# Kernel optimization log

Hardware: AMD Instinct MI355X
Metric: run time of the kernel (lower is better)

## Reference

```python
import jax, jax.numpy as jnp
import numpy as np

DELTA = 0.05
STOP = 10
INV_DELTA = 1.0 / DELTA
TOTAL = int(STOP * INV_DELTA)  # 200 bins
# slice_vol = arange(delta/2, stop, delta)**1 * delta * 2*pi*3
SLICE_VOL = (np.arange(DELTA / 2, STOP, DELTA) * DELTA * 2.0 * np.pi * 3.0).astype(np.float32)


def _cdist(a, b):
    # Euclidean pairwise distance [Na, Nb] via the (a-b)^2 = a^2 + b^2 - 2ab identity
    a2 = jnp.sum(a * a, axis=-1)
    b2 = jnp.sum(b * b, axis=-1)
    d2 = a2[:, None] + b2[None, :] - 2.0 * (a @ b.T)
    return jnp.sqrt(jnp.maximum(d2, 0.0))


def _pair_hist(pa, pb, same, real_size, vol):
    # integer distance bins; torch .int() truncates, distances are >= 0 so floor is equivalent
    bins = jnp.floor(_cdist(pa * real_size, pb * real_size) * INV_DELTA).astype(jnp.int32)
    if same:
        n = pa.shape[0]
        idx = jnp.arange(n)
        bins = bins.at[idx, idx].set(9999)  # fill_diagonal_(9999) -> excluded self-pairs
    valid = (bins < TOTAL).astype(jnp.float32).ravel()  # mask: bins beyond stop dropped
    counts = jnp.zeros(TOTAL, jnp.float32).at[jnp.clip(bins, 0, TOTAL - 1).ravel()].add(valid)
    density = pb.shape[0] / vol
    return counts / density / jnp.asarray(SLICE_VOL) / pa.shape[0]


def setup_inputs() -> dict:
    key = jax.random.key(0)
    k0, k1 = jax.random.split(key)
    pos0 = jax.random.uniform(k0, (4096, 3), dtype=jnp.float32)
    pos1 = jax.random.uniform(k1, (8192, 3), dtype=jnp.float32)
    count = jnp.zeros((2, 2, TOTAL), dtype=jnp.float32)
    real_size = jnp.array([25.0, 25.0, 3.0], dtype=jnp.float32)
    return {"pos0": pos0, "pos1": pos1, "count": count, "real_size": real_size}


def reference(pos0, pos1, count, real_size):
    vol = real_size[0] * real_size[1] * real_size[2]
    pos = [pos0, pos1]
    bufs = [
        jnp.stack([_pair_hist(pos[i], pos[j], i == j, real_size, vol) for j in range(2)])
        for i in range(2)
    ]
    # count buffer is accumulated in-place in torch; return the updated buffer
    return count + jnp.stack(bufs)
```

## Files before the change

kernel.cpp:

```cpp
#include <hip/hip_runtime.h>
#include <math.h>

#define TOTAL 200
#define TB    32
#define BLK   256
#define NW    4
#define GRID  2048
#define NR    16
#define RATIO (BLK/TB)

typedef float f32x4 __attribute__((ext_vector_type(4)));

__global__ void rdf_prep(const float* __restrict__ p0, const float* __restrict__ p1,
                         const float* __restrict__ rs,
                         float4* __restrict__ b0, float4* __restrict__ b1,
                         unsigned int* __restrict__ ghist, int n0, int n1)
{
    const float sx = rs[0], sy = rs[1], sz = rs[2];
    int t = blockIdx.x * blockDim.x + threadIdx.x;
    if (t < n0) {
        float x = p0[t*3+0]*sx, y = p0[t*3+1]*sy, z = p0[t*3+2]*sz;
        b0[t] = make_float4(x, y, z, x*x + y*y + z*z);
    } else if (t < n0 + n1) {
        int u = t - n0;
        float x = p1[u*3+0]*sx, y = p1[u*3+1]*sy, z = p1[u*3+2]*sz;
        b1[u] = make_float4(x, y, z, x*x + y*y + z*z);
    }
    if (t < NR * 3 * TOTAL) ghist[t] = 0;
}

template<bool DIAG>
__device__ __forceinline__ void pair_one(f32x4 q, int J,
                                         float ax, float ay, float az, float a2,
                                         unsigned int* __restrict__ mylh, int ofs)
{
    float dot = ax*q.x + ay*q.y + az*q.z;
    float d2  = (a2 + q.w) - 2.0f*dot;
    float v   = __builtin_amdgcn_sqrtf(fmaxf(d2, 0.0f)) * 20.0f;
    bool ok   = (v < 200.0f);
    if (DIAG) ok = ok && (J > ofs);
    if (ok) atomicAdd(&mylh[(int)v], 1u);
}

template<bool DIAG>
__device__ __forceinline__ void pair_loop(const f32x4* __restrict__ Bb, int colBase,
                                          float ax, float ay, float az, float a2,
                                          unsigned int* __restrict__ mylh, int ofs)
{
    unsigned voff = (unsigned)colBase * 16u;
    #pragma unroll
    for (int jb = 0; jb < TB; jb += 8) {
        f32x4 q0, q1, q2, q3, q4, q5, q6, q7;
        asm volatile(
            "global_load_dwordx4 %0, %8, %9 offset:0\n\t"
            "global_load_dwordx4 %1, %8, %9 offset:16\n\t"
            "global_load_dwordx4 %2, %8, %9 offset:32\n\t"
            "global_load_dwordx4 %3, %8, %9 offset:48\n\t"
            "global_load_dwordx4 %4, %8, %9 offset:64\n\t"
            "global_load_dwordx4 %5, %8, %9 offset:80\n\t"
            "global_load_dwordx4 %6, %8, %9 offset:96\n\t"
            "global_load_dwordx4 %7, %8, %9 offset:112\n\t"
            "s_waitcnt vmcnt(0)"
            : "=&v"(q0), "=&v"(q1), "=&v"(q2), "=&v"(q3),
              "=&v"(q4), "=&v"(q5), "=&v"(q6), "=&v"(q7)
            : "v"(voff), "s"(Bb));
        pair_one<DIAG>(q0, jb+0, ax, ay, az, a2, mylh, ofs);
        pair_one<DIAG>(q1, jb+1, ax, ay, az, a2, mylh, ofs);
        pair_one<DIAG>(q2, jb+2, ax, ay, az, a2, mylh, ofs);
        pair_one<DIAG>(q3, jb+3, ax, ay, az, a2, mylh, ofs);
        pair_one<DIAG>(q4, jb+4, ax, ay, az, a2, mylh, ofs);
        pair_one<DIAG>(q5, jb+5, ax, ay, az, a2, mylh, ofs);
        pair_one<DIAG>(q6, jb+6, ax, ay, az, a2, mylh, ofs);
        pair_one<DIAG>(q7, jb+7, ax, ay, az, a2, mylh, ofs);
        __builtin_amdgcn_sched_barrier(0);
        voff += 128u;
    }
}

__global__ __launch_bounds__(BLK, 8) void rdf_hist(
    const float4* __restrict__ b0, const float4* __restrict__ b1,
    unsigned int* __restrict__ ghist,
    int n0, int n1, int T0, int T01, int Ttot,
    int cb0, int cb1, int rows0, int rows1)
{
    __shared__ unsigned int lh[3][NW][2][TOTAL];

    const int tid  = threadIdx.x;
    const int wave = tid >> 6;
    const int par  = tid & 1;

    uint4* z = (uint4*)lh;
    for (int k = tid; k < 3*NW*2*TOTAL/4; k += BLK) z[k] = make_uint4(0,0,0,0);
    __syncthreads();

    const int gBeg = (int)(((long long)blockIdx.x       * Ttot) / GRID);
    const int gEnd = (int)(((long long)(blockIdx.x + 1) * Ttot) / GRID);

    for (int g = gBeg; g < gEnd; ++g) {
        int type, rb, cb;
        if (g < T0) {
            type = 0; rb = 0;
            while (rb + 1 < rows0 && (cb0*(rb+1) - (RATIO/2)*(rb+1)*rb) <= g) ++rb;
            cb = RATIO*rb + (g - (cb0*rb - (RATIO/2)*rb*(rb-1)));
        } else if (g < T01) {
            int u = g - T0; type = 1; rb = u / cb1; cb = u - rb*cb1;
        } else {
            int u = g - T01; type = 2; rb = 0;
            while (rb + 1 < rows1 && (cb1*(rb+1) - (RATIO/2)*(rb+1)*rb) <= u) ++rb;
            cb = RATIO*rb + (u - (cb1*rb - (RATIO/2)*rb*(rb-1)));
        }
        const float4* Ab = (type == 2) ? b1 : b0;
        const float4* Bb = (type == 0) ? b0 : b1;
        const int nA     = (type == 2) ? n1 : n0;

        const int rowBase = rb * BLK;
        const int colBase = cb * TB;
        const int aIdx    = rowBase + tid;

        float4 a = (aIdx < nA) ? Ab[aIdx]
                               : make_float4(0.f, 0.f, 0.f, 3.0e18f);
        unsigned int* mylh = &lh[type][wave][par][0];
        const f32x4* Bb4   = (const f32x4*)Bb;

        const bool diag = (type != 1) && (colBase < rowBase + BLK);
        if (diag) pair_loop<true >(Bb4, colBase, a.x, a.y, a.z, a.w, mylh, aIdx - colBase);
        else      pair_loop<false>(Bb4, colBase, a.x, a.y, a.z, a.w, mylh, 0);
    }
    __syncthreads();

    unsigned int* gh = ghist + (blockIdx.x & (NR - 1)) * (3 * TOTAL);
    for (int k = tid; k < 3 * TOTAL; k += BLK) {
        int type = k / TOTAL, bin = k - type * TOTAL;
        unsigned int c = 0;
        #pragma unroll
        for (int w = 0; w < NW; ++w)
            { c += lh[type][w][0][bin] + lh[type][w][1][bin]; }
        if (c) atomicAdd(&gh[k], (type == 1) ? c : 2u * c);
    }
}

__global__ void rdf_final(const unsigned int* __restrict__ ghist,
                          const float* __restrict__ count,
                          const float* __restrict__ rs,
                          float* __restrict__ out, int n0, int n1)
{
    int t = blockIdx.x * blockDim.x + threadIdx.x;
    if (t >= 2*2*TOTAL) return;
    int k = t % TOTAL;
    int j = (t / TOTAL) & 1;
    int i = t / (2*TOTAL);

    float vol = rs[0]*rs[1]*rs[2];
    int Na = (i == 0) ? n0 : n1;
    int Nb = (j == 0) ? n0 : n1;
    int hidx = (i == j) ? (i == 0 ? 0 : 2) : 1;

    unsigned int c = 0;
    #pragma unroll
    for (int r = 0; r < NR; ++r) c += ghist[r*3*TOTAL + hidx*TOTAL + k];

    double sv  = ((0.025 + (double)k * 0.05) * 0.05) * 2.0 * M_PI * 3.0;
    float  svf = (float)sv;
    float  density = (float)Nb / vol;
    float  r = (((float)c / density) / svf) / (float)Na;
    out[t] = count[t] + r;
}

extern "C" void kernel_launch(void* const* d_in, const int* in_sizes, int n_in,
                              void* d_out, int out_size, void* d_ws, size_t ws_size,
                              hipStream_t stream) {
    const float* pos0  = (const float*)d_in[0];
    const float* pos1  = (const float*)d_in[1];
    const float* count = (const float*)d_in[2];
    const float* rs    = (const float*)d_in[3];
    float* out = (float*)d_out;

    int n0 = in_sizes[0] / 3;
    int n1 = in_sizes[1] / 3;

    unsigned int* ghist = (unsigned int*)d_ws;
    float4* b0 = (float4*)((char*)d_ws + 40960);
    float4* b1 = b0 + n0;

    int prepBlocks = (n0 + n1 + BLK - 1) / BLK;
    rdf_prep<<<prepBlocks, BLK, 0, stream>>>(pos0, pos1, rs, b0, b1, ghist, n0, n1);

    int rows0 = (n0 + BLK - 1) / BLK;
    int rows1 = (n1 + BLK - 1) / BLK;
    int cb0   = (n0 + TB - 1) / TB;
    int cb1   = (n1 + TB - 1) / TB;
    int T0   = cb0*rows0 - (RATIO/2)*rows0*(rows0-1);
    int Tc   = rows0*cb1;
    int T2   = cb1*rows1 - (RATIO/2)*rows1*(rows1-1);
    int T01  = T0 + Tc;
    int Ttot = T01 + T2;

    rdf_hist<<<GRID, BLK, 0, stream>>>(b0, b1, ghist, n0, n1,
                                       T0, T01, Ttot, cb0, cb1, rows0, rows1);

    rdf_final<<<(2*2*TOTAL + BLK - 1) / BLK, BLK, 0, stream>>>(ghist, count, rs, out, n0, n1);
}
```

Before: 108.0 us.

## Double-buffer column loads, shrink shared histograms, fuse final pass via last-block

The pair loop now software-pipelines global loads in groups of four, waiting with vmcnt(4) so one group's loads overlap the previous group's compute instead of waiting for all eight at once. The per-block shared histogram drops from three type slices to one and is flushed and re-zeroed whenever the work type changes, which shrinks LDS and may raise occupancy at the cost of extra block barriers. The separate finalize kernel is removed: a done-counter lets the last block sum the global histograms and write the output, saving one launch but adding a fence and an atomic per block. The row operand is fetched with inline asm.

```diff
diff --git a/kernel.cpp b/kernel.cpp
--- a/kernel.cpp
+++ b/kernel.cpp
@@ -26,7 +26,7 @@
         float x = p1[u*3+0]*sx, y = p1[u*3+1]*sy, z = p1[u*3+2]*sz;
         b1[u] = make_float4(x, y, z, x*x + y*y + z*z);
     }
-    if (t < NR * 3 * TOTAL) ghist[t] = 0;
+    if (t < NR * 3 * TOTAL + 1) ghist[t] = 0;
 }
 
 template<bool DIAG>
@@ -43,59 +43,109 @@
 }
 
 template<bool DIAG>
+__device__ __forceinline__ void compute4(f32x4 q0, f32x4 q1, f32x4 q2, f32x4 q3, int jb,
+                                         float ax, float ay, float az, float a2,
+                                         unsigned int* __restrict__ mylh, int ofs)
+{
+    pair_one<DIAG>(q0, jb+0, ax, ay, az, a2, mylh, ofs);
+    pair_one<DIAG>(q1, jb+1, ax, ay, az, a2, mylh, ofs);
+    pair_one<DIAG>(q2, jb+2, ax, ay, az, a2, mylh, ofs);
+    pair_one<DIAG>(q3, jb+3, ax, ay, az, a2, mylh, ofs);
+}
+
+#define ISSUE4(q0,q1,q2,q3, o0,o1,o2,o3)                                 \
+    asm volatile(                                                        \
+        "global_load_dwordx4 %0, %4, %5 offset:" o0 "\n\t"               \
+        "global_load_dwordx4 %1, %4, %5 offset:" o1 "\n\t"               \
+        "global_load_dwordx4 %2, %4, %5 offset:" o2 "\n\t"               \
+        "global_load_dwordx4 %3, %4, %5 offset:" o3                      \
+        : "=&v"(q0), "=&v"(q1), "=&v"(q2), "=&v"(q3)                     \
+        : "v"(voff), "s"(Bb))
+
+#define ISSUE4_WAIT4(q0,q1,q2,q3, p0,p1,p2,p3, o0,o1,o2,o3)              \
+    asm volatile(                                                        \
+        "global_load_dwordx4 %0, %8, %9 offset:" o0 "\n\t"               \
+        "global_load_dwordx4 %1, %8, %9 offset:" o1 "\n\t"               \
+        "global_load_dwordx4 %2, %8, %9 offset:" o2 "\n\t"               \
+        "global_load_dwordx4 %3, %8, %9 offset:" o3 "\n\t"               \
+        "s_waitcnt vmcnt(4)"                                             \
+        : "=&v"(q0), "=&v"(q1), "=&v"(q2), "=&v"(q3),                    \
+          "+v"(p0), "+v"(p1), "+v"(p2), "+v"(p3)                         \
+        : "v"(voff), "s"(Bb))
+
+#define WAIT_ALL(p0,p1,p2,p3)                                            \
+    asm volatile("s_waitcnt vmcnt(0)"                                    \
+        : "+v"(p0), "+v"(p1), "+v"(p2), "+v"(p3))
+
+template<bool DIAG>
 __device__ __forceinline__ void pair_loop(const f32x4* __restrict__ Bb, int colBase,
                                           float ax, float ay, float az, float a2,
                                           unsigned int* __restrict__ mylh, int ofs)
 {
     unsigned voff = (unsigned)colBase * 16u;
-    #pragma unroll
-    for (int jb = 0; jb < TB; jb += 8) {
-        f32x4 q0, q1, q2, q3, q4, q5, q6, q7;
-        asm volatile(
-            "global_load_dwordx4 %0, %8, %9 offset:0\n\t"
-            "global_load_dwordx4 %1, %8, %9 offset:16\n\t"
-            "global_load_dwordx4 %2, %8, %9 offset:32\n\t"
-            "global_load_dwordx4 %3, %8, %9 offset:48\n\t"
-            "global_load_dwordx4 %4, %8, %9 offset:64\n\t"
-            "global_load_dwordx4 %5, %8, %9 offset:80\n\t"
-            "global_load_dwordx4 %6, %8, %9 offset:96\n\t"
-            "global_load_dwordx4 %7, %8, %9 offset:112\n\t"
-            "s_waitcnt vmcnt(0)"
-            : "=&v"(q0), "=&v"(q1), "=&v"(q2), "=&v"(q3),
-              "=&v"(q4), "=&v"(q5), "=&v"(q6), "=&v"(q7)
-            : "v"(voff), "s"(Bb));
-        pair_one<DIAG>(q0, jb+0, ax, ay, az, a2, mylh, ofs);
-        pair_one<DIAG>(q1, jb+1, ax, ay, az, a2, mylh, ofs);
-        pair_one<DIAG>(q2, jb+2, ax, ay, az, a2, mylh, ofs);
-        pair_one<DIAG>(q3, jb+3, ax, ay, az, a2, mylh, ofs);
-        pair_one<DIAG>(q4, jb+4, ax, ay, az, a2, mylh, ofs);
-        pair_one<DIAG>(q5, jb+5, ax, ay, az, a2, mylh, ofs);
-        pair_one<DIAG>(q6, jb+6, ax, ay, az, a2, mylh, ofs);
-        pair_one<DIAG>(q7, jb+7, ax, ay, az, a2, mylh, ofs);
-        __builtin_amdgcn_sched_barrier(0);
-        voff += 128u;
-    }
+    f32x4 A0,A1,A2,A3, B0,B1,B2,B3;
+    ISSUE4      (A0,A1,A2,A3,             "0","16","32","48");
+    ISSUE4_WAIT4(B0,B1,B2,B3, A0,A1,A2,A3, "64","80","96","112");
+    compute4<DIAG>(A0,A1,A2,A3,  0, ax,ay,az,a2, mylh, ofs);
+    ISSUE4_WAIT4(A0,A1,A2,A3, B0,B1,B2,B3, "128","144","160","176");
+    compute4<DIAG>(B0,B1,B2,B3,  4, ax,ay,az,a2, mylh, ofs);
+    ISSUE4_WAIT4(B0,B1,B2,B3, A0,A1,A2,A3, "192","208","224","240");
+    compute4<DIAG>(A0,A1,A2,A3,  8, ax,ay,az,a2, mylh, ofs);
+    ISSUE4_WAIT4(A0,A1,A2,A3, B0,B1,B2,B3, "256","272","288","304");
+    compute4<DIAG>(B0,B1,B2,B3, 12, ax,ay,az,a2, mylh, ofs);
+    ISSUE4_WAIT4(B0,B1,B2,B3, A0,A1,A2,A3, "320","336","352","368");
+    compute4<DIAG>(A0,A1,A2,A3, 16, ax,ay,az,a2, mylh, ofs);
+    ISSUE4_WAIT4(A0,A1,A2,A3, B0,B1,B2,B3, "384","400","416","432");
+    compute4<DIAG>(B0,B1,B2,B3, 20, ax,ay,az,a2, mylh, ofs);
+    ISSUE4_WAIT4(B0,B1,B2,B3, A0,A1,A2,A3, "448","464","480","496");
+    compute4<DIAG>(A0,A1,A2,A3, 24, ax,ay,az,a2, mylh, ofs);
+    WAIT_ALL(B0,B1,B2,B3);
+    compute4<DIAG>(B0,B1,B2,B3, 28, ax,ay,az,a2, mylh, ofs);
+}
+
+__device__ __forceinline__ void flush_and_zero(unsigned int (*lh)[2][TOTAL],
+                                               unsigned int* __restrict__ gh,
+                                               int type, int tid)
+{
+    __syncthreads();
+    if (tid < TOTAL) {
+        unsigned int c = 0;
+        #pragma unroll
+        for (int w = 0; w < NW; ++w) c += lh[w][0][tid] + lh[w][1][tid];
+        if (c) atomicAdd(&gh[type*TOTAL + tid], (type == 1) ? c : 2u*c);
+    }
+    __syncthreads();
+    uint4* z = (uint4*)lh;
+    for (int k = tid; k < NW*2*TOTAL/4; k += BLK) z[k] = make_uint4(0,0,0,0);
+    __syncthreads();
 }
 
 __global__ __launch_bounds__(BLK, 8) void rdf_hist(
     const float4* __restrict__ b0, const float4* __restrict__ b1,
-    unsigned int* __restrict__ ghist,
+    unsigned int* __restrict__ ghist, unsigned int* __restrict__ done,
+    const float* __restrict__ count, const float* __restrict__ rs,
+    float* __restrict__ out,
     int n0, int n1, int T0, int T01, int Ttot,
     int cb0, int cb1, int rows0, int rows1)
 {
-    __shared__ unsigned int lh[3][NW][2][TOTAL];
+    __shared__ unsigned int lh[NW][2][TOTAL];
+    __shared__ unsigned int lastFlag;
 
     const int tid  = threadIdx.x;
     const int wave = tid >> 6;
     const int par  = tid & 1;
 
     uint4* z = (uint4*)lh;
-    for (int k = tid; k < 3*NW*2*TOTAL/4; k += BLK) z[k] = make_uint4(0,0,0,0);
-    __syncthreads();
+    for (int k = tid; k < NW*2*TOTAL/4; k += BLK) z[k] = make_uint4(0,0,0,0);
+    __syncthreads();
+
+    unsigned int* gh   = ghist + (blockIdx.x & (NR - 1)) * (3 * TOTAL);
+    unsigned int* mylh = &lh[wave][par][0];
 
     const int gBeg = (int)(((long long)blockIdx.x       * Ttot) / GRID);
     const int gEnd = (int)(((long long)(blockIdx.x + 1) * Ttot) / GRID);
 
+    int curType = -1;
     for (int g = gBeg; g < gEnd; ++g) {
         int type, rb, cb;
         if (g < T0) {
@@ -109,61 +159,56 @@
             while (rb + 1 < rows1 && (cb1*(rb+1) - (RATIO/2)*(rb+1)*rb) <= u) ++rb;
             cb = RATIO*rb + (u - (cb1*rb - (RATIO/2)*rb*(rb-1)));
         }
-        const float4* Ab = (type == 2) ? b1 : b0;
-        const float4* Bb = (type == 0) ? b0 : b1;
-        const int nA     = (type == 2) ? n1 : n0;
+        if (type != curType) {
+            if (curType >= 0) flush_and_zero(lh, gh, curType, tid);
+            curType = type;
+        }
+        const f32x4* Ab = (const f32x4*)((type == 2) ? b1 : b0);
+        const f32x4* Bb = (const f32x4*)((type == 0) ? b0 : b1);
+        const int nA    = (type == 2) ? n1 : n0;
 
         const int rowBase = rb * BLK;
         const int colBase = cb * TB;
         const int aIdx    = rowBase + tid;
 
-        float4 a = (aIdx < nA) ? Ab[aIdx]
-                               : make_float4(0.f, 0.f, 0.f, 3.0e18f);
-        unsigned int* mylh = &lh[type][wave][par][0];
-        const f32x4* Bb4   = (const f32x4*)Bb;
+        int aSafe = (aIdx < nA) ? aIdx : 0;
+        unsigned aoff = (unsigned)aSafe * 16u;
+        f32x4 av;
+        asm volatile("global_load_dwordx4 %0, %1, %2\n\t"
+                     "s_waitcnt vmcnt(0)"
+                     : "=&v"(av) : "v"(aoff), "s"(Ab));
+        float a2 = (aIdx < nA) ? av.w : 3.0e18f;
 
         const bool diag = (type != 1) && (colBase < rowBase + BLK);
-        if (diag) pair_loop<true >(Bb4, colBase, a.x, a.y, a.z, a.w, mylh, aIdx - colBase);
-        else      pair_loop<false>(Bb4, colBase, a.x, a.y, a.z, a.w, mylh, 0);
-    }
-    __syncthreads();
-
-    unsigned int* gh = ghist + (blockIdx.x & (NR - 1)) * (3 * TOTAL);
-    for (int k = tid; k < 3 * TOTAL; k += BLK) {
-        int type = k / TOTAL, bin = k - type * TOTAL;
-        unsigned int c = 0;
-        #pragma unroll
-        for (int w = 0; w < NW; ++w)
-            { c += lh[type][w][0][bin] + lh[type][w][1][bin]; }
-        if (c) atomicAdd(&gh[k], (type == 1) ? c : 2u * c);
-    }
-}
-
-__global__ void rdf_final(const unsigned int* __restrict__ ghist,
-                          const float* __restrict__ count,
-                          const float* __restrict__ rs,
-                          float* __restrict__ out, int n0, int n1)
-{
-    int t = blockIdx.x * blockDim.x + threadIdx.x;
-    if (t >= 2*2*TOTAL) return;
-    int k = t % TOTAL;
-    int j = (t / TOTAL) & 1;
-    int i = t / (2*TOTAL);
-
-    float vol = rs[0]*rs[1]*rs[2];
-    int Na = (i == 0) ? n0 : n1;
-    int Nb = (j == 0) ? n0 : n1;
-    int hidx = (i == j) ? (i == 0 ? 0 : 2) : 1;
-
-    unsigned int c = 0;
-    #pragma unroll
-    for (int r = 0; r < NR; ++r) c += ghist[r*3*TOTAL + hidx*TOTAL + k];
-
-    double sv  = ((0.025 + (double)k * 0.05) * 0.05) * 2.0 * M_PI * 3.0;
-    float  svf = (float)sv;
-    float  density = (float)Nb / vol;
-    float  r = (((float)c / density) / svf) / (float)Na;
-    out[t] = count[t] + r;
+        if (diag) pair_loop<true >(Bb, colBase, av.x, av.y, av.z, a2, mylh, aIdx - colBase);
+        else      pair_loop<false>(Bb, colBase, av.x, av.y, av.z, a2, mylh, 0);
+    }
+    if (curType >= 0) flush_and_zero(lh, gh, curType, tid);
+
+    __threadfence();
+    if (tid == 0) lastFlag = atomicAdd(done, 1u);
+    __syncthreads();
+    if (lastFlag == GRID - 1) {
+        __threadfence();
+        float vol = rs[0]*rs[1]*rs[2];
+        for (int t = tid; t < 2*2*TOTAL; t += BLK) {
+            int k = t % TOTAL;
+            int j = (t / TOTAL) & 1;
+            int i = t / (2*TOTAL);
+            int Na = (i == 0) ? n0 : n1;
+            int Nb = (j == 0) ? n0 : n1;
+            int hidx = (i == j) ? (i == 0 ? 0 : 2) : 1;
+            unsigned int c = 0;
+            #pragma unroll
+            for (int r = 0; r < NR; ++r)
+                c += atomicAdd(&ghist[r*3*TOTAL + hidx*TOTAL + k], 0u);
+            double sv  = ((0.025 + (double)k * 0.05) * 0.05) * 2.0 * M_PI * 3.0;
+            float  svf = (float)sv;
+            float  density = (float)Nb / vol;
+            float  rr = (((float)c / density) / svf) / (float)Na;
+            out[t] = count[t] + rr;
+        }
+    }
 }
 
 extern "C" void kernel_launch(void* const* d_in, const int* in_sizes, int n_in,
@@ -179,6 +224,7 @@
     int n1 = in_sizes[1] / 3;
 
     unsigned int* ghist = (unsigned int*)d_ws;
+    unsigned int* done  = ghist + NR*3*TOTAL;
     float4* b0 = (float4*)((char*)d_ws + 40960);
     float4* b1 = b0 + n0;
 
@@ -195,8 +241,6 @@
     int T01  = T0 + Tc;
     int Ttot = T01 + T2;
 
-    rdf_hist<<<GRID, BLK, 0, stream>>>(b0, b1, ghist, n0, n1,
-                                       T0, T01, Ttot, cb0, cb1, rows0, rows1);
-
-    rdf_final<<<(2*2*TOTAL + BLK - 1) / BLK, BLK, 0, stream>>>(ghist, count, rs, out, n0, n1);
-}
+    rdf_hist<<<GRID, BLK, 0, stream>>>(b0, b1, ghist, done, count, rs, out,
+                                       n0, n1, T0, T01, Ttot, cb0, cb1, rows0, rows1);
+}
```

Result: slower. 203.6 us (+88.6%).
